# Optimization experiments

Hardware: AMD Instinct MI355X
Metric: run time of the kernel (lower is better)

Reference implementation:

```python
import jax, jax.numpy as jnp
import numpy as np

KSIZE = (3, 3, 3)
STRIDE = (2, 2, 2)
PAD = (1, 1, 1)
DIL = (1, 1, 1)


def _box_sum(x):
    # Sum over a (kT,kH,kW) window with stride/padding/dilation, applied over
    # the last 3 dims of a [N, C, T, H, W] tensor (equivalent to conv3d with a
    # ones kernel applied channel-wise).
    return jax.lax.reduce_window(
        x,
        jnp.array(0.0, x.dtype),
        jax.lax.add,
        window_dimensions=(1, 1) + KSIZE,
        window_strides=(1, 1) + STRIDE,
        padding=((0, 0), (0, 0)) + tuple((p, p) for p in PAD),
        window_dilation=(1, 1) + DIL,
    )


def setup_inputs() -> dict:
    key = jax.random.key(0)
    k1, k2 = jax.random.split(key)
    vw = jax.random.normal(k1, (4, 256, 16, 56, 56), dtype=jnp.float32)
    w = jax.random.normal(k2, (4, 16, 256), dtype=jnp.float32)
    return {"vw": vw, "w": w}


def reference(vw, w):
    # vw: [N, C, T, H, W] visual words; w: [N, K, C] language words
    C = vw.shape[1]
    # per-word dot products (the 1x1x1 conv3d in the original): [N, K, T, H, W]
    dotp = jnp.einsum('nkc,ncthw->nkthw', w, vw)
    # aggregate over words (op='max'), keepdim -> [N, 1, T, H, W]
    agg = jnp.max(dotp, axis=1, keepdims=True)
    emap = jnp.exp(agg / np.float32(np.sqrt(C)))
    # box-filter sum of exp map -> denominator [N, 1, T', H', W']
    denom = _box_sum(emap)
    # box-filter sum of exp-weighted features -> numerator [N, C, T', H', W']
    num = _box_sum(vw * emap)
    return num / denom
```

## Files before the change

kernel.cpp:

```cpp
#include <hip/hip_runtime.h>
#include <hip/hip_bf16.h>

#define N_  4
#define C_  256
#define K_  16
#define T_  16
#define H_  56
#define W_  56
#define HW_ (H_ * W_)
#define THW_ (T_ * HW_)
#define TP_ 8
#define HP_ 28
#define WP_ 28
#define PP_ (HP_ * WP_)

__global__ __launch_bounds__(256) void emap_kernel(const float* __restrict__ vw,
                                                   const float* __restrict__ w,
                                                   float* __restrict__ emap) {
    __shared__ float wt[C_ * K_];
    __shared__ float part[8][4][256];

    const int tid  = threadIdx.x;
    const int wv   = tid >> 6;
    const int lane = tid & 63;
    const int bpn  = THW_ / 256;
    const int n    = blockIdx.x / bpn;
    const int s0   = (blockIdx.x % bpn) * 256;

    const float* wn = w + n * (K_ * C_);
#pragma unroll
    for (int k = 0; k < K_; ++k) wt[tid * K_ + k] = wn[k * C_ + tid];
    __syncthreads();

    const float* vbase = vw + (long)(n * C_ + wv * 64) * THW_ + s0 + (lane << 2);

    float a[K_][4];
#pragma unroll
    for (int k = 0; k < K_; ++k)
#pragma unroll
        for (int p = 0; p < 4; ++p) a[k][p] = 0.f;

#pragma unroll 2
    for (int g = 0; g < 16; ++g) {
        float4 vv[4];
#pragma unroll
        for (int j = 0; j < 4; ++j)
            vv[j] = *(const float4*)(vbase + (long)(g * 4 + j) * THW_);
#pragma unroll
        for (int j = 0; j < 4; ++j) {
            const int c = wv * 64 + g * 4 + j;
#pragma unroll
            for (int kk = 0; kk < 4; ++kk) {
                const float4 wk = *(const float4*)&wt[c * K_ + kk * 4];
#define FMA4(Q, WC) \
                a[kk*4+Q][0] += (WC) * vv[j].x; a[kk*4+Q][1] += (WC) * vv[j].y; \
                a[kk*4+Q][2] += (WC) * vv[j].z; a[kk*4+Q][3] += (WC) * vv[j].w;
                FMA4(0, wk.x) FMA4(1, wk.y) FMA4(2, wk.z) FMA4(3, wk.w)
#undef FMA4
            }
        }
    }

    float m = -3.4e38f;
#pragma unroll
    for (int kc = 0; kc < 2; ++kc) {
#pragma unroll
        for (int kq = 0; kq < 8; ++kq) {
            *(float4*)&part[kq][wv][lane * 4] =
                make_float4(a[kc*8+kq][0], a[kc*8+kq][1], a[kc*8+kq][2], a[kc*8+kq][3]);
        }
        __syncthreads();
        float ml = -3.4e38f;
#pragma unroll
        for (int kq = 0; kq < 8; ++kq) {
            const float s = part[kq][0][tid] + part[kq][1][tid]
                          + part[kq][2][tid] + part[kq][3][tid];
            ml = fmaxf(ml, s);
        }
        m = fmaxf(m, ml);
        __syncthreads();
    }

    emap[(long)n * THW_ + s0 + tid] = expf(m * 0.0625f);
}

__global__ __launch_bounds__(256) void rden_kernel(const float* __restrict__ emap,
                                                   float* __restrict__ rden) {
    const int gid = blockIdx.x * 256 + threadIdx.x;
    const int n   = gid / (TP_ * PP_);
    const int r   = gid % (TP_ * PP_);
    const int tp  = r / PP_;
    const int p   = r % PP_;
    const int hp  = p / WP_, wp = p % WP_;
    const int t0  = 2 * tp - 1, h0 = 2 * hp - 1, w0 = 2 * wp - 1;
    const float* eb = emap + (long)n * THW_;

    float den = 0.f;
#pragma unroll
    for (int dt = 0; dt < 3; ++dt) {
        const int tt = t0 + dt;
        const bool tv = (tt >= 0);
        const int tc = tv ? tt : 0;
#pragma unroll
        for (int dh = 0; dh < 3; ++dh) {
            const int h = h0 + dh;
            const bool hv = tv && (h >= 0);
            const int hc = (h >= 0) ? h : 0;
#pragma unroll
            for (int dw = 0; dw < 3; ++dw) {
                const int w = w0 + dw;
                const bool v = hv && (w >= 0);
                const int wc = (w >= 0) ? w : 0;
                const float ev = eb[tc * HW_ + hc * W_ + wc];
                den += v ? ev : 0.f;
            }
        }
    }
    rden[gid] = 1.0f / den;
}

__global__ __launch_bounds__(256) void box_kernel(const float* __restrict__ vw,
                                                  const float* __restrict__ emap,
                                                  const float* __restrict__ rden,
                                                  float* __restrict__ out) {
    __shared__ float sp[3][HW_];
    __shared__ float sr[PP_];

    const int tid = threadIdx.x;
    const int c   = blockIdx.x;
    const int tp  = blockIdx.y;
    const int n   = blockIdx.z;
    const int t0  = 2 * tp - 1;

    const float* eb = emap + (long)n * THW_;
    const float* vb = vw + (long)(n * C_ + c) * THW_;

#pragma unroll
    for (int sl = 0; sl < 3; ++sl) {
        const int tt = t0 + sl;
        if (tt >= 0) {
            const float4* vs = (const float4*)(vb + tt * HW_);
            const float4* es = (const float4*)(eb + tt * HW_);
            for (int i = tid; i < HW_ / 4; i += 256) {
                const float4 v = vs[i], e = es[i];
                *(float4*)&sp[sl][i * 4] =
                    make_float4(v.x * e.x, v.y * e.y, v.z * e.z, v.w * e.w);
            }
        } else {
            for (int i = tid; i < HW_ / 4; i += 256)
                *(float4*)&sp[sl][i * 4] = make_float4(0.f, 0.f, 0.f, 0.f);
        }
    }
    const float* rt = rden + (n * TP_ + tp) * PP_;
    for (int i = tid; i < PP_; i += 256) sr[i] = rt[i];
    __syncthreads();

    float* ob = out + (((long)(n * C_ + c)) * TP_ + tp) * PP_;
    for (int p = tid; p < PP_; p += 256) {
        const int hp = p / WP_, wp = p % WP_;
        const int h0 = 2 * hp - 1, w0 = 2 * wp - 1;
        float num = 0.f;
#pragma unroll
        for (int dh = 0; dh < 3; ++dh) {
            const int h = h0 + dh;
            const bool hv = (h >= 0);
            const int hc = hv ? h : 0;
#pragma unroll
            for (int dw = 0; dw < 3; ++dw) {
                const int w = w0 + dw;
                const bool v = hv && (w >= 0);
                const int wc = (w >= 0) ? w : 0;
                const int o = hc * W_ + wc;
                const float s3 = sp[0][o] + sp[1][o] + sp[2][o];
                num += v ? s3 : 0.f;
            }
        }
        ob[p] = num * sr[p];
    }
}

extern "C" void kernel_launch(void* const* d_in, const int* in_sizes, int n_in,
                              void* d_out, int out_size, void* d_ws, size_t ws_size,
                              hipStream_t stream) {
    const float* vw = (const float*)d_in[0];
    const float* w  = (const float*)d_in[1];
    float* out  = (float*)d_out;
    float* emap = (float*)d_ws;
    float* rden = emap + (long)N_ * THW_;

    emap_kernel<<<784, 256, 0, stream>>>(vw, w, emap);

    rden_kernel<<<98, 256, 0, stream>>>(emap, rden);

    box_kernel<<<dim3(C_, TP_, N_), 256, 0, stream>>>(vw, emap, rden, out);
}
```

Measured before the change: 343.9 us.

## Stream time slices through box kernel ring buffer; reduce emap with shuffles

The box kernel now gives each block one (n,c) pair and walks all output time steps, keeping a 4-slice ring buffer of vw*emap in shared memory. Each input slice is loaded once instead of up to twice, and the next two slices are prefetched into registers while the current step computes. The emap kernel now splits channels across lanes within a wave and combines the partial sums with xor shuffles, which removes the shared-memory reduction and its barriers. The cost is a much smaller grid for the box kernel (1024 blocks), more registers held for prefetch, and shared memory growing to 4 slices.

```diff
diff --git a/kernel.cpp b/kernel.cpp
--- a/kernel.cpp
+++ b/kernel.cpp
@@ -18,11 +18,11 @@
                                                    const float* __restrict__ w,
                                                    float* __restrict__ emap) {
     __shared__ float wt[C_ * K_];
-    __shared__ float part[8][4][256];
-
     const int tid  = threadIdx.x;
+    const int lane = tid & 63;
     const int wv   = tid >> 6;
-    const int lane = tid & 63;
+    const int q    = lane & 3;
+    const int j    = lane >> 2;
     const int bpn  = THW_ / 256;
     const int n    = blockIdx.x / bpn;
     const int s0   = (blockIdx.x % bpn) * 256;
@@ -32,7 +32,7 @@
     for (int k = 0; k < K_; ++k) wt[tid * K_ + k] = wn[k * C_ + tid];
     __syncthreads();
 
-    const float* vbase = vw + (long)(n * C_ + wv * 64) * THW_ + s0 + (lane << 2);
+    const float* vb = vw + (long)(n * C_ + q * 64) * THW_ + s0 + wv * 64 + 4 * j;
 
     float a[K_][4];
 #pragma unroll
@@ -40,48 +40,40 @@
 #pragma unroll
         for (int p = 0; p < 4; ++p) a[k][p] = 0.f;
 
-#pragma unroll 2
-    for (int g = 0; g < 16; ++g) {
-        float4 vv[4];
-#pragma unroll
-        for (int j = 0; j < 4; ++j)
-            vv[j] = *(const float4*)(vbase + (long)(g * 4 + j) * THW_);
-#pragma unroll
-        for (int j = 0; j < 4; ++j) {
-            const int c = wv * 64 + g * 4 + j;
-#pragma unroll
-            for (int kk = 0; kk < 4; ++kk) {
-                const float4 wk = *(const float4*)&wt[c * K_ + kk * 4];
+#pragma unroll 8
+    for (int g = 0; g < 64; ++g) {
+        const float4 v = *(const float4*)(vb + (long)g * THW_);
+        const float* wc = &wt[(q * 64 + g) * K_];
+#pragma unroll
+        for (int kk = 0; kk < 4; ++kk) {
+            const float4 wk = *(const float4*)&wc[kk * 4];
 #define FMA4(Q, WC) \
-                a[kk*4+Q][0] += (WC) * vv[j].x; a[kk*4+Q][1] += (WC) * vv[j].y; \
-                a[kk*4+Q][2] += (WC) * vv[j].z; a[kk*4+Q][3] += (WC) * vv[j].w;
-                FMA4(0, wk.x) FMA4(1, wk.y) FMA4(2, wk.z) FMA4(3, wk.w)
+            a[kk*4+Q][0] += (WC) * v.x; a[kk*4+Q][1] += (WC) * v.y; \
+            a[kk*4+Q][2] += (WC) * v.z; a[kk*4+Q][3] += (WC) * v.w;
+            FMA4(0, wk.x) FMA4(1, wk.y) FMA4(2, wk.z) FMA4(3, wk.w)
 #undef FMA4
-            }
-        }
-    }
+        }
+    }
+
+#pragma unroll
+    for (int k = 0; k < K_; ++k)
+#pragma unroll
+        for (int p = 0; p < 4; ++p) {
+            float t = a[k][p];
+            t += __shfl_xor(t, 1);
+            t += __shfl_xor(t, 2);
+            a[k][p] = t;
+        }
 
     float m = -3.4e38f;
 #pragma unroll
-    for (int kc = 0; kc < 2; ++kc) {
-#pragma unroll
-        for (int kq = 0; kq < 8; ++kq) {
-            *(float4*)&part[kq][wv][lane * 4] =
-                make_float4(a[kc*8+kq][0], a[kc*8+kq][1], a[kc*8+kq][2], a[kc*8+kq][3]);
-        }
-        __syncthreads();
-        float ml = -3.4e38f;
-#pragma unroll
-        for (int kq = 0; kq < 8; ++kq) {
-            const float s = part[kq][0][tid] + part[kq][1][tid]
-                          + part[kq][2][tid] + part[kq][3][tid];
-            ml = fmaxf(ml, s);
-        }
-        m = fmaxf(m, ml);
-        __syncthreads();
-    }
-
-    emap[(long)n * THW_ + s0 + tid] = expf(m * 0.0625f);
+    for (int k = 0; k < K_; ++k) {
+        const float v01 = (q & 1) ? a[k][1] : a[k][0];
+        const float v23 = (q & 1) ? a[k][3] : a[k][2];
+        const float v   = (q & 2) ? v23 : v01;
+        m = fmaxf(m, v);
+    }
+    emap[(long)n * THW_ + s0 + wv * 64 + lane] = expf(m * 0.0625f);
 }
 
 __global__ __launch_bounds__(256) void rden_kernel(const float* __restrict__ emap,
@@ -119,63 +111,99 @@
     rden[gid] = 1.0f / den;
 }
 
+static __device__ __forceinline__ float4 mul4(float4 a, float4 b) {
+    return make_float4(a.x * b.x, a.y * b.y, a.z * b.z, a.w * b.w);
+}
+
 __global__ __launch_bounds__(256) void box_kernel(const float* __restrict__ vw,
                                                   const float* __restrict__ emap,
                                                   const float* __restrict__ rden,
                                                   float* __restrict__ out) {
-    __shared__ float sp[3][HW_];
-    __shared__ float sr[PP_];
+    __shared__ float sp[4][HW_];
 
     const int tid = threadIdx.x;
     const int c   = blockIdx.x;
-    const int tp  = blockIdx.y;
-    const int n   = blockIdx.z;
-    const int t0  = 2 * tp - 1;
-
+    const int n   = blockIdx.y;
+    const float* vb = vw + ((long)(n * C_ + c)) * THW_;
     const float* eb = emap + (long)n * THW_;
-    const float* vb = vw + (long)(n * C_ + c) * THW_;
-
-#pragma unroll
-    for (int sl = 0; sl < 3; ++sl) {
-        const int tt = t0 + sl;
-        if (tt >= 0) {
-            const float4* vs = (const float4*)(vb + tt * HW_);
-            const float4* es = (const float4*)(eb + tt * HW_);
-            for (int i = tid; i < HW_ / 4; i += 256) {
-                const float4 v = vs[i], e = es[i];
-                *(float4*)&sp[sl][i * 4] =
-                    make_float4(v.x * e.x, v.y * e.y, v.z * e.z, v.w * e.w);
+    float* ob = out + ((long)(n * C_ + c)) * (TP_ * PP_);
+    const float* rb = rden + n * (TP_ * PP_);
+
+    {
+        float4* z = (float4*)sp[3];
+        for (int i = tid; i < HW_ / 4; i += 256) z[i] = make_float4(0.f, 0.f, 0.f, 0.f);
+#pragma unroll
+        for (int sl = 0; sl < 2; ++sl) {
+            const float4* vs = (const float4*)(vb + sl * HW_);
+            const float4* es = (const float4*)(eb + sl * HW_);
+            float4* d = (float4*)sp[sl];
+            for (int i = tid; i < HW_ / 4; i += 256) d[i] = mul4(vs[i], es[i]);
+        }
+    }
+    __syncthreads();
+
+    for (int tp = 0; tp < TP_; ++tp) {
+        const int tA = 2 * tp + 2;
+        const bool pf = (tA < T_);
+        float4 pv0, pv1, pv2, pe0, pe1, pe2;
+        float4 qv0, qv1, qv2, qe0, qe1, qe2;
+        if (pf) {
+            const float4* vA = (const float4*)(vb + tA * HW_);
+            const float4* eA = (const float4*)(eb + tA * HW_);
+            const float4* vB = (const float4*)(vb + (tA + 1) * HW_);
+            const float4* eB = (const float4*)(eb + (tA + 1) * HW_);
+            pv0 = vA[tid]; pv1 = vA[tid + 256]; pv2 = vA[tid + 512];
+            pe0 = eA[tid]; pe1 = eA[tid + 256]; pe2 = eA[tid + 512];
+            qv0 = vB[tid]; qv1 = vB[tid + 256]; qv2 = vB[tid + 512];
+            qe0 = eB[tid]; qe1 = eB[tid + 256]; qe2 = eB[tid + 512];
+        }
+
+        const float* sA = sp[(2 * tp + 3) & 3];
+        const float* sB = sp[(2 * tp) & 3];
+        const float* sC = sp[(2 * tp + 1) & 3];
+        const float* rt = rb + tp * PP_;
+        float* ot = ob + tp * PP_;
+        for (int p = tid; p < PP_; p += 256) {
+            const int hp = p / WP_, wp = p % WP_;
+            const int h0 = 2 * hp - 1;
+            const int wE = 2 * wp;
+            const int wO = (wp > 0) ? (2 * wp - 1) : 0;
+            float num = 0.f;
+#pragma unroll
+            for (int dh = 0; dh < 3; ++dh) {
+                const int h = h0 + dh;
+                const int base = ((h >= 0) ? h : 0) * W_;
+                const float e0 = sA[base + wO] + sB[base + wO] + sC[base + wO];
+                const float2 a2 = *(const float2*)&sA[base + wE];
+                const float2 b2 = *(const float2*)&sB[base + wE];
+                const float2 c2 = *(const float2*)&sC[base + wE];
+                float row = a2.x + a2.y + b2.x + b2.y + c2.x + c2.y;
+                row += (wp > 0) ? e0 : 0.f;
+                num += (h >= 0) ? row : 0.f;
             }
-        } else {
-            for (int i = tid; i < HW_ / 4; i += 256)
-                *(float4*)&sp[sl][i * 4] = make_float4(0.f, 0.f, 0.f, 0.f);
-        }
-    }
-    const float* rt = rden + (n * TP_ + tp) * PP_;
-    for (int i = tid; i < PP_; i += 256) sr[i] = rt[i];
-    __syncthreads();
-
-    float* ob = out + (((long)(n * C_ + c)) * TP_ + tp) * PP_;
-    for (int p = tid; p < PP_; p += 256) {
-        const int hp = p / WP_, wp = p % WP_;
-        const int h0 = 2 * hp - 1, w0 = 2 * wp - 1;
-        float num = 0.f;
-#pragma unroll
-        for (int dh = 0; dh < 3; ++dh) {
-            const int h = h0 + dh;
-            const bool hv = (h >= 0);
-            const int hc = hv ? h : 0;
-#pragma unroll
-            for (int dw = 0; dw < 3; ++dw) {
-                const int w = w0 + dw;
-                const bool v = hv && (w >= 0);
-                const int wc = (w >= 0) ? w : 0;
-                const int o = hc * W_ + wc;
-                const float s3 = sp[0][o] + sp[1][o] + sp[2][o];
-                num += v ? s3 : 0.f;
+            ot[p] = num * rt[p];
+        }
+        __syncthreads();
+
+        if (pf) {
+            float4* dA = (float4*)sp[tA & 3];
+            float4* dB = (float4*)sp[(tA + 1) & 3];
+            dA[tid]       = mul4(pv0, pe0);
+            dA[tid + 256] = mul4(pv1, pe1);
+            dA[tid + 512] = mul4(pv2, pe2);
+            dB[tid]       = mul4(qv0, qe0);
+            dB[tid + 256] = mul4(qv1, qe1);
+            dB[tid + 512] = mul4(qv2, qe2);
+            if (tid < 16) {
+                const float4* vA = (const float4*)(vb + tA * HW_);
+                const float4* eA = (const float4*)(eb + tA * HW_);
+                const float4* vB = (const float4*)(vb + (tA + 1) * HW_);
+                const float4* eB = (const float4*)(eb + (tA + 1) * HW_);
+                dA[768 + tid] = mul4(vA[768 + tid], eA[768 + tid]);
+                dB[768 + tid] = mul4(vB[768 + tid], eB[768 + tid]);
             }
         }
-        ob[p] = num * sr[p];
+        __syncthreads();
     }
 }
 
@@ -192,5 +220,5 @@
 
     rden_kernel<<<98, 256, 0, stream>>>(emap, rden);
 
-    box_kernel<<<dim3(C_, TP_, N_), 256, 0, stream>>>(vw, emap, rden, out);
-}
+    box_kernel<<<dim3(C_, N_), 256, 0, stream>>>(vw, emap, rden, out);
+}
```

Result: slower. 385.5 us (+12.1%).
